# Kernel optimization log

Hardware: AMD Instinct MI355X
Metric: run time of the kernel (lower is better)

Reference implementation:

```python
import jax, jax.numpy as jnp
import numpy as np

BS, L, D, N = 4, 2048, 1024, 16

def setup_inputs() -> dict:
    key = jax.random.key(0)
    ks = jax.random.split(key, 8)
    s = 1.0 / np.sqrt(D)
    x  = jax.random.normal(ks[0], (BS, L, D), dtype=jnp.float32)
    # torch Linear params; stored transposed so y = x @ W + b
    W1 = jax.random.uniform(ks[1], (D, D), jnp.float32, -s, s)
    b1 = jax.random.uniform(ks[2], (D,),   jnp.float32, -s, s)
    W2 = jax.random.uniform(ks[3], (D, N), jnp.float32, -s, s)
    b2 = jax.random.uniform(ks[4], (N,),   jnp.float32, -s, s)
    W3 = jax.random.uniform(ks[5], (D, N), jnp.float32, -s, s)
    b3 = jax.random.uniform(ks[6], (N,),   jnp.float32, -s, s)
    A  = jax.random.normal(ks[7], (D, N),  jnp.float32) * np.sqrt(2.0 / (D + N))  # xavier
    return {"x": x, "W1": W1, "b1": b1, "W2": W2, "b2": b2, "W3": W3, "b3": b3, "A": A}

def reference(x, W1, b1, W2, b2, W3, b3, A):
    # S6 forward (non-recurrent branch).
    B = x @ W2 + b2                     # (b,l,n)
    C = x @ W3 + b3                     # (b,l,n)
    delta = jax.nn.softplus(x @ W1 + b1)  # (b,l,d)
    # dA = exp(einsum('bld,dn->bldn', delta, A)) is multiplied by an all-zero h
    # in the original forward, so it does not affect the output (dead code under DCE).
    dB = jnp.einsum('bld,bln->bldn', delta, B)   # (b,l,d,n) -- 512 MB intermediate
    h = x[..., None] * dB                         # (b,l,d,n)
    y = jnp.einsum('bln,bldn->bld', C, h)         # (b,l,d)
    return y
```

## Files before the change

kernel.cpp:

```cpp
#include <hip/hip_runtime.h>
#include <hip/hip_bf16.h>
#include <math.h>


namespace {

constexpr int Dd   = 1024;
constexpr int ROWS = 8192;

typedef __bf16 bf16x8 __attribute__((ext_vector_type(8)));
typedef float  floatx4 __attribute__((ext_vector_type(4)));

#define LDS_BAR() asm volatile("s_waitcnt lgkmcnt(0)\n\ts_barrier" ::: "memory")

__device__ __forceinline__ float softplus_fast(float v) {
    float l = __logf(1.0f + __expf(v));
    return v > 15.0f ? v : l;
}
__device__ __forceinline__ float bf_lo(unsigned short u) {
    union { unsigned q; float f; } c; c.q = ((unsigned)u) << 16; return c.f;
}

__global__ __launch_bounds__(256) void w23_kernel(
    const float* __restrict__ W2, const float* __restrict__ W3,
    __bf16* __restrict__ W2t, __bf16* __restrict__ W3t)
{
    const int t  = threadIdx.x;
    const int n  = t >> 4;
    const int k0 = blockIdx.x * 64 + (t & 15) * 4;
    ushort4 a, b;
    union { __bf16 h; unsigned short u; } c;
    c.h = (__bf16)W2[(size_t)(k0 + 0) * 16 + n]; a.x = c.u;
    c.h = (__bf16)W2[(size_t)(k0 + 1) * 16 + n]; a.y = c.u;
    c.h = (__bf16)W2[(size_t)(k0 + 2) * 16 + n]; a.z = c.u;
    c.h = (__bf16)W2[(size_t)(k0 + 3) * 16 + n]; a.w = c.u;
    c.h = (__bf16)W3[(size_t)(k0 + 0) * 16 + n]; b.x = c.u;
    c.h = (__bf16)W3[(size_t)(k0 + 1) * 16 + n]; b.y = c.u;
    c.h = (__bf16)W3[(size_t)(k0 + 2) * 16 + n]; b.z = c.u;
    c.h = (__bf16)W3[(size_t)(k0 + 3) * 16 + n]; b.w = c.u;
    *(ushort4*)&W2t[(size_t)n * Dd + k0] = a;
    *(ushort4*)&W3t[(size_t)n * Dd + k0] = b;
}

__global__ __launch_bounds__(256, 4) void prep_kernel(
    const float* __restrict__ X, const float* __restrict__ W1,
    const __bf16* __restrict__ W2t, const float* __restrict__ b2,
    const __bf16* __restrict__ W3t, const float* __restrict__ b3,
    __bf16* __restrict__ Xb, __bf16* __restrict__ W1t, float* __restrict__ Sv)
{
    const int t = threadIdx.x;

    if (blockIdx.x >= 512) {
        __shared__ __bf16 tile[64][66];
        const int bidx = blockIdx.x - 512;
        const int bi = bidx >> 4, bj = bidx & 15;
        const int c = t & 63, r4 = t >> 6;
        #pragma unroll
        for (int i = 0; i < 16; ++i) {
            const int r = i * 4 + r4;
            tile[r][c] = (__bf16)W1[(size_t)(bi * 64 + r) * Dd + bj * 64 + c];
        }
        __syncthreads();
        #pragma unroll
        for (int i = 0; i < 16; ++i) {
            const int r = i * 4 + r4;
            W1t[(size_t)(bj * 64 + r) * Dd + bi * 64 + c] = tile[c][r];
        }
        return;
    }

    __shared__ float red[4][2][16][16];
    const int w = t >> 6, lane = t & 63;
    const int l15 = lane & 15, quad = lane >> 4;
    const int row0 = blockIdx.x * 16;
    const int kw = w * 256;
    const size_t xoff = (size_t)(row0 + l15) * Dd;
    const size_t woff = (size_t)l15 * Dd;

    floatx4 acc0 = {0.f, 0.f, 0.f, 0.f}, acc1 = {0.f, 0.f, 0.f, 0.f};
    #pragma unroll
    for (int ks = 0; ks < 8; ++ks) {
        const int k0 = kw + ks * 32 + quad * 8;
        const float4 xa = *(const float4*)&X[xoff + k0];
        const float4 xb = *(const float4*)&X[xoff + k0 + 4];
        bf16x8 af;
        af[0] = (__bf16)xa.x; af[1] = (__bf16)xa.y;
        af[2] = (__bf16)xa.z; af[3] = (__bf16)xa.w;
        af[4] = (__bf16)xb.x; af[5] = (__bf16)xb.y;
        af[6] = (__bf16)xb.z; af[7] = (__bf16)xb.w;
        *(bf16x8*)&Xb[xoff + k0] = af;
        const bf16x8 w2f = *(const bf16x8*)&W2t[woff + k0];
        const bf16x8 w3f = *(const bf16x8*)&W3t[woff + k0];
        acc0 = __builtin_amdgcn_mfma_f32_16x16x32_bf16(af, w2f, acc0, 0, 0, 0);
        acc1 = __builtin_amdgcn_mfma_f32_16x16x32_bf16(af, w3f, acc1, 0, 0, 0);
    }
    #pragma unroll
    for (int r = 0; r < 4; ++r) {
        red[w][0][quad * 4 + r][l15] = acc0[r];
        red[w][1][quad * 4 + r][l15] = acc1[r];
    }
    __syncthreads();
    {
        const int r = t >> 4, n = t & 15;
        float B = b2[n], C = b3[n];
        #pragma unroll
        for (int ww = 0; ww < 4; ++ww) {
            B += red[ww][0][r][n];
            C += red[ww][1][r][n];
        }
        float p = B * C;
        p += __shfl_xor(p, 1); p += __shfl_xor(p, 2);
        p += __shfl_xor(p, 4); p += __shfl_xor(p, 8);
        if (n == 0) Sv[row0 + r] = p;
    }
}

__global__ __launch_bounds__(256, 2) void gemm_kernel(
    const __bf16* __restrict__ Xb, const __bf16* __restrict__ W1t,
    const float* __restrict__ Sv, const float* __restrict__ b1,
    float* __restrict__ Y)
{
    __shared__ __attribute__((aligned(16))) __bf16 lds[8192];
    const int t = threadIdx.x, lane = t & 63;
    const int w = t >> 6, wm = w & 1, wn = w >> 1;
    const int l15 = lane & 15, quad = lane >> 4;
    const int cb = blockIdx.x & 7, rb = blockIdx.x >> 3;
    const int row0 = rb * 128, col0 = cb * 128;

    floatx4 acc[4][4] = {};

    const __bf16* gA[2]; const __bf16* gB[2];
    int dA[2], dB[2];
    #pragma unroll
    for (int r = 0; r < 2; ++r) {
        const int u = r * 256 + t;
        const int p = u >> 3, s = u & 7, c4 = s ^ (p & 7);
        const int rowL = 2 * p + (c4 >> 2), chk = c4 & 3;
        gA[r] = Xb  + (size_t)(row0 + rowL) * Dd + chk * 8;
        gB[r] = W1t + (size_t)(col0 + rowL) * Dd + chk * 8;
        dA[r] = u * 8;
        dB[r] = 4096 + u * 8;
    }

    bf16x8 bufA[2][2], bufB[2][2];

    auto gload = [&](int buf, int k) {
        #pragma unroll
        for (int r = 0; r < 2; ++r) {
            bufA[buf][r] = *(const bf16x8*)(gA[r] + k);
            bufB[buf][r] = *(const bf16x8*)(gB[r] + k);
        }
    };
    auto store_lds = [&](int buf) {
        #pragma unroll
        for (int r = 0; r < 2; ++r) {
            *(bf16x8*)&lds[dA[r]] = bufA[buf][r];
            *(bf16x8*)&lds[dB[r]] = bufB[buf][r];
        }
    };
    auto compute = [&]() {
        bf16x8 af[4], bfr[4];
        #pragma unroll
        for (int mt = 0; mt < 4; ++mt) {
            const int rl = wm * 64 + mt * 16 + l15;
            const int p = rl >> 1, c4 = ((rl & 1) << 2) | quad, s = c4 ^ (p & 7);
            af[mt] = *(const bf16x8*)&lds[p * 64 + s * 8];
        }
        #pragma unroll
        for (int nt = 0; nt < 4; ++nt) {
            const int nl = wn * 64 + nt * 16 + l15;
            const int p = nl >> 1, c4 = ((nl & 1) << 2) | quad, s = c4 ^ (p & 7);
            bfr[nt] = *(const bf16x8*)&lds[4096 + p * 64 + s * 8];
        }
        #pragma unroll
        for (int mt = 0; mt < 4; ++mt)
            #pragma unroll
            for (int nt = 0; nt < 4; ++nt)
                acc[mt][nt] = __builtin_amdgcn_mfma_f32_16x16x32_bf16(
                    af[mt], bfr[nt], acc[mt][nt], 0, 0, 0);
    };

    gload(0, 0);
    for (int k0 = 0; k0 < Dd; k0 += 64) {
        gload(1, k0 + 32);
        LDS_BAR();
        store_lds(0);
        LDS_BAR();
        compute();
        if (k0 + 64 < Dd) gload(0, k0 + 64);
        LDS_BAR();
        store_lds(1);
        LDS_BAR();
        compute();
    }

    float bias[4];
    #pragma unroll
    for (int nt = 0; nt < 4; ++nt) bias[nt] = b1[col0 + wn * 64 + nt * 16 + l15];

    #pragma unroll
    for (int mt = 0; mt < 4; ++mt) {
        #pragma unroll
        for (int rr = 0; rr < 4; ++rr) {
            const int row = row0 + wm * 64 + mt * 16 + quad * 4 + rr;
            const float sv = Sv[row];
            const unsigned short* xrow =
                (const unsigned short*)(Xb + (size_t)row * Dd + col0);
            float* yrow = Y + (size_t)row * Dd + col0;
            #pragma unroll
            for (int nt = 0; nt < 4; ++nt) {
                const int cl = wn * 64 + nt * 16 + l15;
                const float v  = acc[mt][nt][rr] + bias[nt];
                const float sp = softplus_fast(v);
                yrow[cl] = bf_lo(xrow[cl]) * sp * sv;
            }
        }
    }
}

}

extern "C" void kernel_launch(void* const* d_in, const int* in_sizes, int n_in,
                              void* d_out, int out_size, void* d_ws, size_t ws_size,
                              hipStream_t stream)
{
    const float* X  = (const float*)d_in[0];
    const float* W1 = (const float*)d_in[1];
    const float* b1 = (const float*)d_in[2];
    const float* W2 = (const float*)d_in[3];
    const float* b2 = (const float*)d_in[4];
    const float* W3 = (const float*)d_in[5];
    const float* b3 = (const float*)d_in[6];
    float* Y = (float*)d_out;

    char* ws = (char*)d_ws;
    __bf16* Xb  = (__bf16*)ws;
    __bf16* W1t = (__bf16*)(ws + 16777216);
    float*  Sv  = (float*) (ws + 16777216 + 2097152);
    __bf16* W2t = (__bf16*)(ws + 16777216 + 2097152 + 32768);
    __bf16* W3t = (__bf16*)(ws + 16777216 + 2097152 + 65536);

    hipLaunchKernelGGL(w23_kernel, dim3(16), dim3(256), 0, stream, W2, W3, W2t, W3t);
    hipLaunchKernelGGL(prep_kernel, dim3(768), dim3(256), 0, stream,
                       X, W1, W2t, b2, W3t, b3, Xb, W1t, Sv);
    hipLaunchKernelGGL(gemm_kernel, dim3((ROWS / 128) * (Dd / 128)), dim3(256), 0, stream,
                       Xb, W1t, Sv, b1, Y);
}
```

Measured before the change: 134.3 us.

## Stage GEMM tiles via direct global-to-LDS loads with double-buffered K=64 steps

Replaces the register-staged global loads and LDS stores in the W1 GEMM with direct global_load_lds transfers into a double-buffered LDS ring. Each stage now covers K=64 per tile with a simpler XOR swizzle, and the loop uses vmcnt-based waits so the next stage's loads overlap the current compute. The aim is to cut VGPR pressure, the extra LDS-store instructions and the number of barriers per K step. In exchange, LDS use per block grows to 64 KB, which may limit occupancy. Correctness depends on the wait counts matching the number of outstanding loads.

```diff
diff --git a/kernel.cpp b/kernel.cpp
--- a/kernel.cpp
+++ b/kernel.cpp
@@ -11,14 +11,18 @@
 typedef __bf16 bf16x8 __attribute__((ext_vector_type(8)));
 typedef float  floatx4 __attribute__((ext_vector_type(4)));
 
-#define LDS_BAR() asm volatile("s_waitcnt lgkmcnt(0)\n\ts_barrier" ::: "memory")
-
 __device__ __forceinline__ float softplus_fast(float v) {
     float l = __logf(1.0f + __expf(v));
     return v > 15.0f ? v : l;
 }
 __device__ __forceinline__ float bf_lo(unsigned short u) {
     union { unsigned q; float f; } c; c.q = ((unsigned)u) << 16; return c.f;
+}
+
+__device__ __forceinline__ void gld_lds16(const __bf16* g, __bf16* l) {
+    __builtin_amdgcn_global_load_lds(
+        (const __attribute__((address_space(1))) void*)g,
+        (__attribute__((address_space(3))) void*)l, 16, 0, 0);
 }
 
 __global__ __launch_bounds__(256) void w23_kernel(
@@ -120,7 +124,7 @@
     const float* __restrict__ Sv, const float* __restrict__ b1,
     float* __restrict__ Y)
 {
-    __shared__ __attribute__((aligned(16))) __bf16 lds[8192];
+    __shared__ __attribute__((aligned(16))) __bf16 lds[32768];
     const int t = threadIdx.x, lane = t & 63;
     const int w = t >> 6, wm = w & 1, wn = w >> 1;
     const int l15 = lane & 15, quad = lane >> 4;
@@ -129,70 +133,63 @@
 
     floatx4 acc[4][4] = {};
 
-    const __bf16* gA[2]; const __bf16* gB[2];
-    int dA[2], dB[2];
-    #pragma unroll
-    for (int r = 0; r < 2; ++r) {
-        const int u = r * 256 + t;
-        const int p = u >> 3, s = u & 7, c4 = s ^ (p & 7);
-        const int rowL = 2 * p + (c4 >> 2), chk = c4 & 3;
-        gA[r] = Xb  + (size_t)(row0 + rowL) * Dd + chk * 8;
-        gB[r] = W1t + (size_t)(col0 + rowL) * Dd + chk * 8;
-        dA[r] = u * 8;
-        dB[r] = 4096 + u * 8;
-    }
-
-    bf16x8 bufA[2][2], bufB[2][2];
-
-    auto gload = [&](int buf, int k) {
-        #pragma unroll
-        for (int r = 0; r < 2; ++r) {
-            bufA[buf][r] = *(const bf16x8*)(gA[r] + k);
-            bufB[buf][r] = *(const bf16x8*)(gB[r] + k);
+    const __bf16* gA[4]; const __bf16* gB[4];
+    int dA[4], dB[4];
+    #pragma unroll
+    for (int i = 0; i < 4; ++i) {
+        const int u = i * 256 + t;
+        const int r = u >> 3;
+        const int c = (u & 7) ^ (r & 7);
+        gA[i] = Xb  + (size_t)(row0 + r) * Dd + c * 8;
+        gB[i] = W1t + (size_t)(col0 + r) * Dd + c * 8;
+        dA[i] = u * 8;
+        dB[i] = 16384 + u * 8;
+    }
+
+    auto stage = [&](int buf, int k) {
+        #pragma unroll
+        for (int i = 0; i < 4; ++i) {
+            gld_lds16(gA[i] + k, &lds[buf * 8192 + dA[i]]);
+            gld_lds16(gB[i] + k, &lds[buf * 8192 + dB[i]]);
         }
     };
-    auto store_lds = [&](int buf) {
-        #pragma unroll
-        for (int r = 0; r < 2; ++r) {
-            *(bf16x8*)&lds[dA[r]] = bufA[buf][r];
-            *(bf16x8*)&lds[dB[r]] = bufB[buf][r];
+
+    auto compute = [&](int buf) {
+        const __bf16* Al = &lds[buf * 8192];
+        const __bf16* Bl = &lds[16384 + buf * 8192];
+        #pragma unroll
+        for (int ks = 0; ks < 2; ++ks) {
+            const int sA = ((ks << 2) | quad) ^ (l15 & 7);
+            bf16x8 af[4], bfr[4];
+            #pragma unroll
+            for (int mt = 0; mt < 4; ++mt)
+                af[mt] = *(const bf16x8*)&Al[(wm * 64 + mt * 16 + l15) * 64 + sA * 8];
+            #pragma unroll
+            for (int nt = 0; nt < 4; ++nt)
+                bfr[nt] = *(const bf16x8*)&Bl[(wn * 64 + nt * 16 + l15) * 64 + sA * 8];
+            #pragma unroll
+            for (int mt = 0; mt < 4; ++mt)
+                #pragma unroll
+                for (int nt = 0; nt < 4; ++nt)
+                    acc[mt][nt] = __builtin_amdgcn_mfma_f32_16x16x32_bf16(
+                        af[mt], bfr[nt], acc[mt][nt], 0, 0, 0);
         }
     };
-    auto compute = [&]() {
-        bf16x8 af[4], bfr[4];
-        #pragma unroll
-        for (int mt = 0; mt < 4; ++mt) {
-            const int rl = wm * 64 + mt * 16 + l15;
-            const int p = rl >> 1, c4 = ((rl & 1) << 2) | quad, s = c4 ^ (p & 7);
-            af[mt] = *(const bf16x8*)&lds[p * 64 + s * 8];
-        }
-        #pragma unroll
-        for (int nt = 0; nt < 4; ++nt) {
-            const int nl = wn * 64 + nt * 16 + l15;
-            const int p = nl >> 1, c4 = ((nl & 1) << 2) | quad, s = c4 ^ (p & 7);
-            bfr[nt] = *(const bf16x8*)&lds[4096 + p * 64 + s * 8];
-        }
-        #pragma unroll
-        for (int mt = 0; mt < 4; ++mt)
-            #pragma unroll
-            for (int nt = 0; nt < 4; ++nt)
-                acc[mt][nt] = __builtin_amdgcn_mfma_f32_16x16x32_bf16(
-                    af[mt], bfr[nt], acc[mt][nt], 0, 0, 0);
-    };
-
-    gload(0, 0);
-    for (int k0 = 0; k0 < Dd; k0 += 64) {
-        gload(1, k0 + 32);
-        LDS_BAR();
-        store_lds(0);
-        LDS_BAR();
-        compute();
-        if (k0 + 64 < Dd) gload(0, k0 + 64);
-        LDS_BAR();
-        store_lds(1);
-        LDS_BAR();
-        compute();
-    }
+
+    stage(0, 0);
+    #pragma unroll 1
+    for (int k0 = 0; k0 < Dd - 64; k0 += 64) {
+        const int cur = (k0 >> 6) & 1;
+        stage(cur ^ 1, k0 + 64);
+        asm volatile("s_waitcnt vmcnt(8)" ::: "memory");
+        __builtin_amdgcn_s_barrier();
+        compute(cur);
+        asm volatile("s_waitcnt lgkmcnt(0)" ::: "memory");
+        __builtin_amdgcn_s_barrier();
+    }
+    asm volatile("s_waitcnt vmcnt(0)" ::: "memory");
+    __builtin_amdgcn_s_barrier();
+    compute(((Dd >> 6) - 1) & 1);
 
     float bias[4];
     #pragma unroll
```

Result: faster. 131.6 us (-2.0%).
